# Optimization experiments

Measured on AMD Instinct MI355X. Metric: run time of the kernel, lower is better.

Reference implementation:

```python
import jax, jax.numpy as jnp
import numpy as np

B, L, D, O = 4, 256, 512, 128

def setup_inputs() -> dict:
    key = jax.random.key(0)
    k1, k2, k3, k4, k5, k6 = jax.random.split(key, 6)
    return {
        "x1": jax.random.normal(k1, (B, L, D), jnp.float32),
        "x2": jax.random.normal(k2, (B, L, D), jnp.float32),
        "bw": jax.random.uniform(k3, (2,), jnp.float32),
        "W_bil": jax.random.normal(k4, (O, D + 1, D + 1), jnp.float32) * 0.02,
        "W_lin": jax.random.normal(k5, (2 * D, O), jnp.float32) * 0.02,
        "b_lin": jax.random.normal(k6, (O,), jnp.float32) * 0.02,
    }

def reference(x1, x2, bw, W_bil, W_lin, b_lin):
    bwn = jax.nn.softmax(bw)
    d1 = x1.shape[-1]
    # Bilinear with bias_x/bias_y: append ones column to x1 and x2.
    ones1 = jnp.ones((*x1.shape[:2], 1), x1.dtype)
    ones2 = jnp.ones((*x2.shape[:2], 1), x2.dtype)
    x1b = jnp.concatenate([x1, ones1], axis=-1)  # [B, L1, D+1]
    x2b = jnp.concatenate([x2, ones2], axis=-1)  # [B, L2, D+1]
    # einsum 'bxi,oij,byj->boxy' then permute(0,2,3,1) -> bxyo
    bilinear_logits = jnp.einsum('bxi,oij,byj->bxyo', x1b, W_bil, x2b)
    # linear over concat([x1 expanded, x2 expanded]) == split-weight broadcast sum
    lin1 = x1 @ W_lin[:d1]   # [B, L1, O]
    lin2 = x2 @ W_lin[d1:]   # [B, L2, O]
    linear_logits = lin1[:, :, None, :] + lin2[:, None, :, :] + b_lin  # [B, L1, L2, O]
    return bwn[0] * bilinear_logits + bwn[1] * linear_logits
```

## Files before the change

### kernel.cpp

```cpp
#include <hip/hip_runtime.h>


#define LL 256
#define DD 512
#define OO 128
#define BB 4
#define WB_OI 263169
#define WB_R512 262656

typedef __attribute__((ext_vector_type(8))) short  short8;
typedef __attribute__((ext_vector_type(8))) unsigned short us8;
typedef __attribute__((ext_vector_type(4))) unsigned short us4;
typedef __attribute__((ext_vector_type(4))) float  f32x4;

__device__ __forceinline__ unsigned short f2bf(float f) {
    unsigned int u = __builtin_bit_cast(unsigned int, f);
    u = (u + 0x7FFFu + ((u >> 16) & 1u)) >> 16;
    return (unsigned short)u;
}
__device__ __forceinline__ float bf2f(unsigned short s) {
    return __builtin_bit_cast(float, (unsigned int)s << 16);
}
__device__ __forceinline__ void load_lds16(const void* g, void* l) {
    __builtin_amdgcn_global_load_lds(
        (const __attribute__((address_space(1))) unsigned int*)g,
        (__attribute__((address_space(3))) unsigned int*)l, 16, 0, 0);
}

__global__ __launch_bounds__(256) void cast2_kernel(
    const float* __restrict__ x1, const float* __restrict__ x2,
    unsigned short* __restrict__ x1b, unsigned short* __restrict__ x2b)
{
    int i = blockIdx.x * 256 + threadIdx.x;
    const float* s; unsigned short* d; int j;
    if (i < 131072) { s = x1; d = x1b; j = i; }
    else            { s = x2; d = x2b; j = i - 131072; }
    float4 v = ((const float4*)s)[j];
    us4 u; u.x = f2bf(v.x); u.y = f2bf(v.y); u.z = f2bf(v.z); u.w = f2bf(v.w);
    *(us4*)(d + (size_t)j * 4) = u;
}

__global__ __launch_bounds__(256) void prepw_kernel(
    const float* __restrict__ Wb, const float* __restrict__ bw,
    unsigned short* __restrict__ Wb16)
{
    const int t = threadIdx.x;
    const int row = blockIdx.x * 4 + (t >> 6);
    const int o = row >> 9, i = row & 511;
    const int l = t & 63;
    const float e0 = __expf(bw[0]), e1 = __expf(bw[1]);
    const float bwn0 = e0 / (e0 + e1);
    const float* src = Wb + (size_t)o * WB_OI + (size_t)i * 513;
    unsigned short* dst = Wb16 + (size_t)row * 512;
    float v[8];
    #pragma unroll
    for (int e = 0; e < 8; ++e) v[e] = src[e * 64 + l];
    #pragma unroll
    for (int e = 0; e < 8; ++e) dst[e * 64 + l] = f2bf(bwn0 * v[e]);
}

__global__ __launch_bounds__(256) void prep512_kernel(
    const float* __restrict__ Wb, float* __restrict__ W512T)
{
    int idx = blockIdx.x * 256 + threadIdx.x;
    if (idx < 513 * 128) {
        const int o = idx & 127, j = idx >> 7;
        W512T[idx] = Wb[(size_t)o * WB_OI + WB_R512 + j];
    }
}

__global__ __launch_bounds__(128) void u512_kernel(
    const float* __restrict__ x2, const float* __restrict__ W512T,
    const float* __restrict__ W_lin, const float* __restrict__ b_lin,
    const float* __restrict__ bw, float* __restrict__ u512buf)
{
    __shared__ float xs[DD];
    const int by = blockIdx.x;
    const int o  = threadIdx.x;
    const float* xr = x2 + (size_t)by * DD;
    for (int j = o; j < DD; j += 128) xs[j] = xr[j];
    __syncthreads();
    float s1 = W512T[512 * 128 + o];
    float s2 = b_lin[o];
    #pragma unroll 4
    for (int j = 0; j < DD; ++j) {
        s1 += xs[j] * W512T[j * 128 + o];
        s2 += xs[j] * W_lin[(size_t)(DD + j) * OO + o];
    }
    const float e0 = __expf(bw[0]), e1 = __expf(bw[1]);
    const float bwn0 = e0 / (e0 + e1), bwn1 = e1 / (e0 + e1);
    u512buf[(size_t)by * OO + o] = bwn0 * s1 + bwn1 * s2;
}

__global__ __launch_bounds__(256) void passA_kernel(
    const unsigned short* __restrict__ x2b, const unsigned short* __restrict__ Wb16,
    const float* __restrict__ W_bil, const float* __restrict__ W_lin,
    const float* __restrict__ bw, unsigned short* __restrict__ Up)
{
    __shared__ __align__(16) char smem[33280];
    unsigned short* As0 = (unsigned short*)smem;
    unsigned short* Bs0 = (unsigned short*)(smem + 8192);
    unsigned short* As1 = (unsigned short*)(smem + 16384);
    unsigned short* Bs1 = (unsigned short*)(smem + 24576);
    unsigned short* Cs  = (unsigned short*)smem;
    float* corr = (float*)(smem + 32768);

    const int t = threadIdx.x, w = t >> 6, l = t & 63;
    const int ib = blockIdx.x * 128;
    const int yg = blockIdx.y * 128;
    const int o  = blockIdx.z;
    const int wy = w & 1, wx = w >> 1;

    f32x4 acc[4][4] = {};
    const unsigned short* Wo16 = Wb16 + (size_t)o * DD * DD;

    const int rb0 = w * 32;
    const int rr  = l >> 2;
    const int kof = (l & 3) * 8;

#define STAGE_A(ASP, BSP, K0) do {                                              \
    _Pragma("unroll")                                                           \
    for (int q = 0; q < 2; ++q) {                                               \
        const int rb = rb0 + q * 16, rrow = rb + rr, ko = (K0) + kof;           \
        load_lds16(x2b  + (size_t)(yg + rrow) * DD + ko, (ASP) + rb * 32);      \
        load_lds16(Wo16 + (size_t)(ib + rrow) * DD + ko, (BSP) + rb * 32);      \
    } } while (0)

    STAGE_A(As0, Bs0, 0);
    __syncthreads();

    const int mrow = wy * 64 + (l & 15);
    const int ncol = wx * 64 + (l & 15);
    const int kg = (l >> 4) * 8;

    #pragma unroll 2
    for (int kt = 0; kt < 16; ++kt) {
        const int cur = kt & 1;
        unsigned short* Asr = cur ? As1 : As0;
        unsigned short* Bsr = cur ? Bs1 : Bs0;
        unsigned short* Asn = cur ? As0 : As1;
        unsigned short* Bsn = cur ? Bs0 : Bs1;
        if (kt < 15) STAGE_A(Asn, Bsn, (kt + 1) * 32);
        short8 af[4], bfr[4];
        #pragma unroll
        for (int mt = 0; mt < 4; ++mt) af[mt]  = *(const short8*)(Asr + (mrow + mt * 16) * 32 + kg);
        #pragma unroll
        for (int nt = 0; nt < 4; ++nt) bfr[nt] = *(const short8*)(Bsr + (ncol + nt * 16) * 32 + kg);
        #pragma unroll
        for (int mt = 0; mt < 4; ++mt)
            #pragma unroll
            for (int nt = 0; nt < 4; ++nt)
                acc[mt][nt] = __builtin_amdgcn_mfma_f32_16x16x32_bf16(af[mt], bfr[nt], acc[mt][nt], 0, 0, 0);
        __syncthreads();
    }
#undef STAGE_A

    const float e0 = __expf(bw[0]), e1 = __expf(bw[1]);
    const float bwn0 = e0 / (e0 + e1), bwn1 = e1 / (e0 + e1);
    if (t < 128) {
        const int ig = ib + t;
        corr[t] = bwn1 * W_lin[(size_t)ig * OO + o]
                + bwn0 * W_bil[(size_t)o * WB_OI + (size_t)ig * 513 + 512];
    }
    #pragma unroll
    for (int half = 0; half < 2; ++half) {
        if (wy == half) {
            #pragma unroll
            for (int mt = 0; mt < 4; ++mt) {
                const int yl = mt * 16 + ((l >> 4) << 2);
                #pragma unroll
                for (int nt = 0; nt < 4; ++nt) {
                    const int ic = wx * 64 + nt * 16 + (l & 15);
                    #pragma unroll
                    for (int r = 0; r < 4; ++r)
                        Cs[(yl + r) * 136 + ic] = f2bf(acc[mt][nt][r]);
                }
            }
        }
        __syncthreads();
        #pragma unroll
        for (int p = 0; p < 4; ++p) {
            const int yl = p * 16 + (t >> 4);
            const int i0 = (t & 15) * 8;
            short8 v = *(const short8*)(Cs + yl * 136 + i0);
            us8 uo;
            #pragma unroll
            for (int e = 0; e < 8; ++e)
                uo[e] = f2bf(bf2f((unsigned short)v[e]) + corr[i0 + e]);
            *(us8*)(Up + ((size_t)(yg + half * 64 + yl) * OO + o) * DD + ib + i0) = uo;
        }
        __syncthreads();
    }
}

__global__ __launch_bounds__(256) void passB_kernel(
    const unsigned short* __restrict__ x1b, const unsigned short* __restrict__ Up,
    const float* __restrict__ u512buf, float* __restrict__ out)
{
    __shared__ __align__(16) char smem[33280];
    unsigned short* As0 = (unsigned short*)smem;
    unsigned short* Bs0 = (unsigned short*)(smem + 8192);
    unsigned short* As1 = (unsigned short*)(smem + 16384);
    unsigned short* Bs1 = (unsigned short*)(smem + 24576);
    float* u5 = (float*)(smem + 32768);

    const int t = threadIdx.x, w = t >> 6, l = t & 63;
    const int xb = blockIdx.x * 128;
    const int yg = blockIdx.y;
    const int bb = yg >> 8, y = yg & 255;
    const int wy = w & 1, wx = w >> 1;
    if (t < 128) u5[t] = u512buf[(size_t)yg * OO + t];

    f32x4 acc[4][4] = {};

    const int rb0 = w * 32;
    const int rr  = l >> 2;
    const int kof = (l & 3) * 8;

#define STAGE_B(ASP, BSP, K0) do {                                                   \
    _Pragma("unroll")                                                                \
    for (int q = 0; q < 2; ++q) {                                                    \
        const int rb = rb0 + q * 16, rrow = rb + rr, ko = (K0) + kof;                \
        load_lds16(x1b + (size_t)(bb * LL + xb + rrow) * DD + ko, (ASP) + rb * 32);  \
        load_lds16(Up  + (size_t)(yg * OO + rrow) * DD + ko,      (BSP) + rb * 32);  \
    } } while (0)

    STAGE_B(As0, Bs0, 0);
    __syncthreads();

    const int mrow = wy * 64 + (l & 15);
    const int ncol = wx * 64 + (l & 15);
    const int kg = (l >> 4) * 8;

    #pragma unroll 2
    for (int kt = 0; kt < 16; ++kt) {
        const int cur = kt & 1;
        unsigned short* Asr = cur ? As1 : As0;
        unsigned short* Bsr = cur ? Bs1 : Bs0;
        unsigned short* Asn = cur ? As0 : As1;
        unsigned short* Bsn = cur ? Bs0 : Bs1;
        if (kt < 15) STAGE_B(Asn, Bsn, (kt + 1) * 32);
        short8 af[4], bfr[4];
        #pragma unroll
        for (int mt = 0; mt < 4; ++mt) af[mt]  = *(const short8*)(Asr + (mrow + mt * 16) * 32 + kg);
        #pragma unroll
        for (int nt = 0; nt < 4; ++nt) bfr[nt] = *(const short8*)(Bsr + (ncol + nt * 16) * 32 + kg);
        #pragma unroll
        for (int mt = 0; mt < 4; ++mt)
            #pragma unroll
            for (int nt = 0; nt < 4; ++nt)
                acc[mt][nt] = __builtin_amdgcn_mfma_f32_16x16x32_bf16(af[mt], bfr[nt], acc[mt][nt], 0, 0, 0);
        __syncthreads();
    }
#undef STAGE_B

    #pragma unroll
    for (int mt = 0; mt < 4; ++mt) {
        const int xr = wy * 64 + mt * 16 + ((l >> 4) << 2);
        #pragma unroll
        for (int nt = 0; nt < 4; ++nt) {
            const int oc = wx * 64 + nt * 16 + (l & 15);
            const float c = u5[oc];
            #pragma unroll
            for (int r = 0; r < 4; ++r)
                out[((size_t)(bb * LL + xb + xr + r) * LL + y) * OO + oc] = acc[mt][nt][r] + c;
        }
    }
}

extern "C" void kernel_launch(void* const* d_in, const int* in_sizes, int n_in,
                              void* d_out, int out_size, void* d_ws, size_t ws_size,
                              hipStream_t stream)
{
    const float* x1    = (const float*)d_in[0];
    const float* x2    = (const float*)d_in[1];
    const float* bw    = (const float*)d_in[2];
    const float* W_bil = (const float*)d_in[3];
    const float* W_lin = (const float*)d_in[4];
    const float* b_lin = (const float*)d_in[5];
    float* out = (float*)d_out;

    char* ws = (char*)d_ws;
    unsigned short* x1b16 = (unsigned short*)ws;
    unsigned short* x2b16 = (unsigned short*)(ws + (1u << 20));
    float*          u512b = (float*)(ws + (2u << 20));
    float*          W512T = (float*)(ws + (2u << 20) + (512u << 10));
    unsigned short* Wb16  = (unsigned short*)(ws + (3u << 20));
    unsigned short* Up    = (unsigned short*)(ws + (3u << 20) + ((size_t)128 * 512 * 512 * 2));

    cast2_kernel<<<1024, 256, 0, stream>>>(x1, x2, x1b16, x2b16);
    prepw_kernel<<<16384, 256, 0, stream>>>(W_bil, bw, Wb16);
    prep512_kernel<<<257, 256, 0, stream>>>(W_bil, W512T);
    u512_kernel<<<BB * LL, 128, 0, stream>>>(x2, W512T, W_lin, b_lin, bw, u512b);

    passA_kernel<<<dim3(4, 8, OO), 256, 0, stream>>>(x2b16, Wb16, W_bil, W_lin, bw, Up);
    passB_kernel<<<dim3(2, BB * LL), 256, 0, stream>>>(x1b16, Up, u512b, out);
}
```

Measured before the change: 479.8 us.

## Quad-buffer GEMM pipelines with swizzled LDS, setprio, and XCD-aware block remap

```diff
diff --git a/kernel.cpp b/kernel.cpp
--- a/kernel.cpp
+++ b/kernel.cpp
@@ -97,18 +97,16 @@
     const float* __restrict__ W_bil, const float* __restrict__ W_lin,
     const float* __restrict__ bw, unsigned short* __restrict__ Up)
 {
-    __shared__ __align__(16) char smem[33280];
-    unsigned short* As0 = (unsigned short*)smem;
-    unsigned short* Bs0 = (unsigned short*)(smem + 8192);
-    unsigned short* As1 = (unsigned short*)(smem + 16384);
-    unsigned short* Bs1 = (unsigned short*)(smem + 24576);
+    __shared__ __align__(16) char smem[65536];
     unsigned short* Cs  = (unsigned short*)smem;
-    float* corr = (float*)(smem + 32768);
+    float* corr = (float*)(smem + 17408);
 
     const int t = threadIdx.x, w = t >> 6, l = t & 63;
-    const int ib = blockIdx.x * 128;
-    const int yg = blockIdx.y * 128;
-    const int o  = blockIdx.z;
+    const int id  = blockIdx.x;
+    const int lin = (id & 7) * 512 + (id >> 3);
+    const int o   = lin >> 5;
+    const int ib  = (lin & 3) * 128;
+    const int yg  = ((lin >> 2) & 7) * 128;
     const int wy = w & 1, wx = w >> 1;
 
     f32x4 acc[4][4] = {};
@@ -116,45 +114,60 @@
 
     const int rb0 = w * 32;
     const int rr  = l >> 2;
-    const int kof = (l & 3) * 8;
-
-#define STAGE_A(ASP, BSP, K0) do {                                              \
+    const int kof = ((l & 3) ^ ((l >> 3) & 3)) * 8;
+
+#define STAGE_A(S, K0) do {                                                     \
+    unsigned short* As_ = (unsigned short*)(smem + (S) * 16384);                \
+    unsigned short* Bs_ = As_ + 4096;                                           \
     _Pragma("unroll")                                                           \
     for (int q = 0; q < 2; ++q) {                                               \
         const int rb = rb0 + q * 16, rrow = rb + rr, ko = (K0) + kof;           \
-        load_lds16(x2b  + (size_t)(yg + rrow) * DD + ko, (ASP) + rb * 32);      \
-        load_lds16(Wo16 + (size_t)(ib + rrow) * DD + ko, (BSP) + rb * 32);      \
+        load_lds16(x2b  + (size_t)(yg + rrow) * DD + ko, As_ + rb * 32);        \
+        load_lds16(Wo16 + (size_t)(ib + rrow) * DD + ko, Bs_ + rb * 32);        \
     } } while (0)
 
-    STAGE_A(As0, Bs0, 0);
-    __syncthreads();
+    STAGE_A(0, 0); STAGE_A(1, 32); STAGE_A(2, 64);
 
     const int mrow = wy * 64 + (l & 15);
     const int ncol = wx * 64 + (l & 15);
-    const int kg = (l >> 4) * 8;
-
-    #pragma unroll 2
-    for (int kt = 0; kt < 16; ++kt) {
-        const int cur = kt & 1;
-        unsigned short* Asr = cur ? As1 : As0;
-        unsigned short* Bsr = cur ? Bs1 : Bs0;
-        unsigned short* Asn = cur ? As0 : As1;
-        unsigned short* Bsn = cur ? Bs0 : Bs1;
-        if (kt < 15) STAGE_A(Asn, Bsn, (kt + 1) * 32);
-        short8 af[4], bfr[4];
-        #pragma unroll
-        for (int mt = 0; mt < 4; ++mt) af[mt]  = *(const short8*)(Asr + (mrow + mt * 16) * 32 + kg);
-        #pragma unroll
-        for (int nt = 0; nt < 4; ++nt) bfr[nt] = *(const short8*)(Bsr + (ncol + nt * 16) * 32 + kg);
-        #pragma unroll
-        for (int mt = 0; mt < 4; ++mt)
-            #pragma unroll
-            for (int nt = 0; nt < 4; ++nt)
-                acc[mt][nt] = __builtin_amdgcn_mfma_f32_16x16x32_bf16(af[mt], bfr[nt], acc[mt][nt], 0, 0, 0);
-        __syncthreads();
-    }
+    const int psel = ((l >> 4) ^ ((l >> 1) & 3)) * 8;
+
+#define COMPUTE_T(S) do {                                                       \
+    const unsigned short* As_ = (const unsigned short*)(smem + (S) * 16384);    \
+    const unsigned short* Bs_ = As_ + 4096;                                     \
+    short8 af[4], bfr[4];                                                       \
+    _Pragma("unroll")                                                           \
+    for (int mt = 0; mt < 4; ++mt) af[mt]  = *(const short8*)(As_ + (mrow + mt * 16) * 32 + psel); \
+    _Pragma("unroll")                                                           \
+    for (int nt = 0; nt < 4; ++nt) bfr[nt] = *(const short8*)(Bs_ + (ncol + nt * 16) * 32 + psel); \
+    __builtin_amdgcn_s_setprio(1);                                              \
+    _Pragma("unroll")                                                           \
+    for (int mt = 0; mt < 4; ++mt)                                              \
+        _Pragma("unroll")                                                       \
+        for (int nt = 0; nt < 4; ++nt)                                          \
+            acc[mt][nt] = __builtin_amdgcn_mfma_f32_16x16x32_bf16(af[mt], bfr[nt], acc[mt][nt], 0, 0, 0); \
+    __builtin_amdgcn_s_setprio(0);                                              \
+  } while (0)
+
+    #pragma unroll
+    for (int kt = 0; kt < 14; ++kt) {
+        asm volatile("s_waitcnt vmcnt(8)" ::: "memory");
+        __builtin_amdgcn_s_barrier();
+        asm volatile("" ::: "memory");
+        if (kt < 13) STAGE_A((kt + 3) & 3, (kt + 3) * 32);
+        COMPUTE_T(kt & 3);
+    }
+    asm volatile("s_waitcnt vmcnt(4)" ::: "memory");
+    __builtin_amdgcn_s_barrier();
+    asm volatile("" ::: "memory");
+    COMPUTE_T(2);
+    asm volatile("s_waitcnt vmcnt(0)" ::: "memory");
+    __builtin_amdgcn_s_barrier();
+    asm volatile("" ::: "memory");
+    COMPUTE_T(3);
 #undef STAGE_A
 
+    __syncthreads();
     const float e0 = __expf(bw[0]), e1 = __expf(bw[1]);
     const float bwn0 = e0 / (e0 + e1), bwn1 = e1 / (e0 + e1);
     if (t < 128) {
@@ -197,61 +210,52 @@
     const unsigned short* __restrict__ x1b, const unsigned short* __restrict__ Up,
     const float* __restrict__ u512buf, float* __restrict__ out)
 {
-    __shared__ __align__(16) char smem[33280];
-    unsigned short* As0 = (unsigned short*)smem;
-    unsigned short* Bs0 = (unsigned short*)(smem + 8192);
-    unsigned short* As1 = (unsigned short*)(smem + 16384);
-    unsigned short* Bs1 = (unsigned short*)(smem + 24576);
-    float* u5 = (float*)(smem + 32768);
+    __shared__ __align__(16) char smem[65536];
 
     const int t = threadIdx.x, w = t >> 6, l = t & 63;
     const int xb = blockIdx.x * 128;
     const int yg = blockIdx.y;
     const int bb = yg >> 8, y = yg & 255;
     const int wy = w & 1, wx = w >> 1;
-    if (t < 128) u5[t] = u512buf[(size_t)yg * OO + t];
 
     f32x4 acc[4][4] = {};
 
     const int rb0 = w * 32;
     const int rr  = l >> 2;
-    const int kof = (l & 3) * 8;
-
-#define STAGE_B(ASP, BSP, K0) do {                                                   \
+    const int kof = ((l & 3) ^ ((l >> 3) & 3)) * 8;
+
+#define STAGE_B(S, K0) do {                                                          \
+    unsigned short* As_ = (unsigned short*)(smem + (S) * 16384);                     \
+    unsigned short* Bs_ = As_ + 4096;                                                \
     _Pragma("unroll")                                                                \
     for (int q = 0; q < 2; ++q) {                                                    \
         const int rb = rb0 + q * 16, rrow = rb + rr, ko = (K0) + kof;                \
-        load_lds16(x1b + (size_t)(bb * LL + xb + rrow) * DD + ko, (ASP) + rb * 32);  \
-        load_lds16(Up  + (size_t)(yg * OO + rrow) * DD + ko,      (BSP) + rb * 32);  \
+        load_lds16(x1b + (size_t)(bb * LL + xb + rrow) * DD + ko, As_ + rb * 32);    \
+        load_lds16(Up  + (size_t)(yg * OO + rrow) * DD + ko,      Bs_ + rb * 32);    \
     } } while (0)
 
-    STAGE_B(As0, Bs0, 0);
-    __syncthreads();
+    STAGE_B(0, 0); STAGE_B(1, 32); STAGE_B(2, 64);
 
     const int mrow = wy * 64 + (l & 15);
     const int ncol = wx * 64 + (l & 15);
-    const int kg = (l >> 4) * 8;
-
-    #pragma unroll 2
-    for (int kt = 0; kt < 16; ++kt) {
-        const int cur = kt & 1;
-        unsigned short* Asr = cur ? As1 : As0;
-        unsigned short* Bsr = cur ? Bs1 : Bs0;
-        unsigned short* Asn = cur ? As0 : As1;
-        unsigned short* Bsn = cur ? Bs0 : Bs1;
-        if (kt < 15) STAGE_B(Asn, Bsn, (kt + 1) * 32);
-        short8 af[4], bfr[4];
-        #pragma unroll
-        for (int mt = 0; mt < 4; ++mt) af[mt]  = *(const short8*)(Asr + (mrow + mt * 16) * 32 + kg);
-        #pragma unroll
-        for (int nt = 0; nt < 4; ++nt) bfr[nt] = *(const short8*)(Bsr + (ncol + nt * 16) * 32 + kg);
-        #pragma unroll
-        for (int mt = 0; mt < 4; ++mt)
-            #pragma unroll
-            for (int nt = 0; nt < 4; ++nt)
-                acc[mt][nt] = __builtin_amdgcn_mfma_f32_16x16x32_bf16(af[mt], bfr[nt], acc[mt][nt], 0, 0, 0);
-        __syncthreads();
-    }
+    const int psel = ((l >> 4) ^ ((l >> 1) & 3)) * 8;
+
+    #pragma unroll
+    for (int kt = 0; kt < 14; ++kt) {
+        asm volatile("s_waitcnt vmcnt(8)" ::: "memory");
+        __builtin_amdgcn_s_barrier();
+        asm volatile("" ::: "memory");
+        if (kt < 13) STAGE_B((kt + 3) & 3, (kt + 3) * 32);
+        COMPUTE_T(kt & 3);
+    }
+    asm volatile("s_waitcnt vmcnt(4)" ::: "memory");
+    __builtin_amdgcn_s_barrier();
+    asm volatile("" ::: "memory");
+    COMPUTE_T(2);
+    asm volatile("s_waitcnt vmcnt(0)" ::: "memory");
+    __builtin_amdgcn_s_barrier();
+    asm volatile("" ::: "memory");
+    COMPUTE_T(3);
 #undef STAGE_B
 
     #pragma unroll
@@ -260,7 +264,7 @@
         #pragma unroll
         for (int nt = 0; nt < 4; ++nt) {
             const int oc = wx * 64 + nt * 16 + (l & 15);
-            const float c = u5[oc];
+            const float c = u512buf[(size_t)yg * OO + oc];
             #pragma unroll
             for (int r = 0; r < 4; ++r)
                 out[((size_t)(bb * LL + xb + xr + r) * LL + y) * OO + oc] = acc[mt][nt][r] + c;
@@ -293,6 +297,6 @@
     prep512_kernel<<<257, 256, 0, stream>>>(W_bil, W512T);
     u512_kernel<<<BB * LL, 128, 0, stream>>>(x2, W512T, W_lin, b_lin, bw, u512b);
 
-    passA_kernel<<<dim3(4, 8, OO), 256, 0, stream>>>(x2b16, Wb16, W_bil, W_lin, bw, Up);
+    passA_kernel<<<4096, 256, 0, stream>>>(x2b16, Wb16, W_bil, W_lin, bw, Up);
     passB_kernel<<<dim3(2, BB * LL), 256, 0, stream>>>(x1b16, Up, u512b, out);
 }
```

Result: no change. 488.5 us (+1.8%).

## Swizzle LDS tiles, remap passA block order, retile passB to 256x64

Applied to the files above, without the earlier changes.

```diff
diff --git a/kernel.cpp b/kernel.cpp
--- a/kernel.cpp
+++ b/kernel.cpp
@@ -106,9 +106,11 @@
     float* corr = (float*)(smem + 32768);
 
     const int t = threadIdx.x, w = t >> 6, l = t & 63;
-    const int ib = blockIdx.x * 128;
-    const int yg = blockIdx.y * 128;
-    const int o  = blockIdx.z;
+    const int id  = blockIdx.x;
+    const int lin = (id & 7) * 512 + (id >> 3);
+    const int o   = lin >> 5;
+    const int ib  = (lin & 3) * 128;
+    const int yg  = ((lin >> 2) & 7) * 128;
     const int wy = w & 1, wx = w >> 1;
 
     f32x4 acc[4][4] = {};
@@ -116,14 +118,15 @@
 
     const int rb0 = w * 32;
     const int rr  = l >> 2;
-    const int kof = (l & 3) * 8;
-
-#define STAGE_A(ASP, BSP, K0) do {                                              \
+    const int csw = ((l & 3) ^ (rr & 3)) * 8;
+
+#define STAGE_A(AS_, BS_, K0) do {                                              \
     _Pragma("unroll")                                                           \
     for (int q = 0; q < 2; ++q) {                                               \
-        const int rb = rb0 + q * 16, rrow = rb + rr, ko = (K0) + kof;           \
-        load_lds16(x2b  + (size_t)(yg + rrow) * DD + ko, (ASP) + rb * 32);      \
-        load_lds16(Wo16 + (size_t)(ib + rrow) * DD + ko, (BSP) + rb * 32);      \
+        const int rb = rb0 + q * 16;                                            \
+        const int grow = rb + rr;                                               \
+        load_lds16(x2b  + (size_t)(yg + grow) * DD + (K0) + csw, (AS_) + rb * 32); \
+        load_lds16(Wo16 + (size_t)(ib + grow) * DD + (K0) + csw, (BS_) + rb * 32); \
     } } while (0)
 
     STAGE_A(As0, Bs0, 0);
@@ -131,7 +134,7 @@
 
     const int mrow = wy * 64 + (l & 15);
     const int ncol = wx * 64 + (l & 15);
-    const int kg = (l >> 4) * 8;
+    const int psel = ((l >> 4) ^ (l & 3)) * 8;
 
     #pragma unroll 2
     for (int kt = 0; kt < 16; ++kt) {
@@ -143,9 +146,9 @@
         if (kt < 15) STAGE_A(Asn, Bsn, (kt + 1) * 32);
         short8 af[4], bfr[4];
         #pragma unroll
-        for (int mt = 0; mt < 4; ++mt) af[mt]  = *(const short8*)(Asr + (mrow + mt * 16) * 32 + kg);
-        #pragma unroll
-        for (int nt = 0; nt < 4; ++nt) bfr[nt] = *(const short8*)(Bsr + (ncol + nt * 16) * 32 + kg);
+        for (int mt = 0; mt < 4; ++mt) af[mt]  = *(const short8*)(Asr + (mrow + mt * 16) * 32 + psel);
+        #pragma unroll
+        for (int nt = 0; nt < 4; ++nt) bfr[nt] = *(const short8*)(Bsr + (ncol + nt * 16) * 32 + psel);
         #pragma unroll
         for (int mt = 0; mt < 4; ++mt)
             #pragma unroll
@@ -197,54 +200,50 @@
     const unsigned short* __restrict__ x1b, const unsigned short* __restrict__ Up,
     const float* __restrict__ u512buf, float* __restrict__ out)
 {
-    __shared__ __align__(16) char smem[33280];
-    unsigned short* As0 = (unsigned short*)smem;
-    unsigned short* Bs0 = (unsigned short*)(smem + 8192);
-    unsigned short* As1 = (unsigned short*)(smem + 16384);
-    unsigned short* Bs1 = (unsigned short*)(smem + 24576);
-    float* u5 = (float*)(smem + 32768);
+    __shared__ __align__(16) char smem[40960];
 
     const int t = threadIdx.x, w = t >> 6, l = t & 63;
-    const int xb = blockIdx.x * 128;
+    const int ob = blockIdx.x;
     const int yg = blockIdx.y;
     const int bb = yg >> 8, y = yg & 255;
-    const int wy = w & 1, wx = w >> 1;
-    if (t < 128) u5[t] = u512buf[(size_t)yg * OO + t];
 
     f32x4 acc[4][4] = {};
-
-    const int rb0 = w * 32;
+    const unsigned short* Abase = x1b + (size_t)bb * LL * DD;
+    const unsigned short* Bbase = Up + ((size_t)yg * OO + ob * 64) * DD;
+
     const int rr  = l >> 2;
-    const int kof = (l & 3) * 8;
-
-#define STAGE_B(ASP, BSP, K0) do {                                                   \
-    _Pragma("unroll")                                                                \
-    for (int q = 0; q < 2; ++q) {                                                    \
-        const int rb = rb0 + q * 16, rrow = rb + rr, ko = (K0) + kof;                \
-        load_lds16(x1b + (size_t)(bb * LL + xb + rrow) * DD + ko, (ASP) + rb * 32);  \
-        load_lds16(Up  + (size_t)(yg * OO + rrow) * DD + ko,      (BSP) + rb * 32);  \
-    } } while (0)
-
-    STAGE_B(As0, Bs0, 0);
+    const int csw = ((l & 3) ^ (rr & 3)) * 8;
+
+#define STAGE_B(S, K0) do {                                                     \
+    unsigned short* As_ = (unsigned short*)(smem + (S) * 20480);                \
+    unsigned short* Bs_ = As_ + 8192;                                           \
+    _Pragma("unroll")                                                           \
+    for (int q = 0; q < 4; ++q) {                                               \
+        const int seg = q * 4 + w;                          \
+        load_lds16(Abase + (size_t)(seg * 16 + rr) * DD + (K0) + csw,           \
+                   As_ + seg * 512);                                            \
+    }                                                                           \
+    load_lds16(Bbase + (size_t)(w * 16 + rr) * DD + (K0) + csw, Bs_ + w * 512); \
+  } while (0)
+
+    STAGE_B(0, 0);
     __syncthreads();
 
-    const int mrow = wy * 64 + (l & 15);
-    const int ncol = wx * 64 + (l & 15);
-    const int kg = (l >> 4) * 8;
+    const int mrow = w * 64 + (l & 15);
+    const int ncol = l & 15;
+    const int psel = ((l >> 4) ^ (l & 3)) * 8;
 
     #pragma unroll 2
     for (int kt = 0; kt < 16; ++kt) {
         const int cur = kt & 1;
-        unsigned short* Asr = cur ? As1 : As0;
-        unsigned short* Bsr = cur ? Bs1 : Bs0;
-        unsigned short* Asn = cur ? As0 : As1;
-        unsigned short* Bsn = cur ? Bs0 : Bs1;
-        if (kt < 15) STAGE_B(Asn, Bsn, (kt + 1) * 32);
+        if (kt < 15) STAGE_B(cur ^ 1, (kt + 1) * 32);
+        const unsigned short* As_ = (const unsigned short*)(smem + cur * 20480);
+        const unsigned short* Bs_ = As_ + 8192;
         short8 af[4], bfr[4];
         #pragma unroll
-        for (int mt = 0; mt < 4; ++mt) af[mt]  = *(const short8*)(Asr + (mrow + mt * 16) * 32 + kg);
-        #pragma unroll
-        for (int nt = 0; nt < 4; ++nt) bfr[nt] = *(const short8*)(Bsr + (ncol + nt * 16) * 32 + kg);
+        for (int mt = 0; mt < 4; ++mt) af[mt]  = *(const short8*)(As_ + (mrow + mt * 16) * 32 + psel);
+        #pragma unroll
+        for (int nt = 0; nt < 4; ++nt) bfr[nt] = *(const short8*)(Bs_ + (ncol + nt * 16) * 32 + psel);
         #pragma unroll
         for (int mt = 0; mt < 4; ++mt)
             #pragma unroll
@@ -255,15 +254,15 @@
 #undef STAGE_B
 
     #pragma unroll
-    for (int mt = 0; mt < 4; ++mt) {
-        const int xr = wy * 64 + mt * 16 + ((l >> 4) << 2);
-        #pragma unroll
-        for (int nt = 0; nt < 4; ++nt) {
-            const int oc = wx * 64 + nt * 16 + (l & 15);
-            const float c = u5[oc];
+    for (int nt = 0; nt < 4; ++nt) {
+        const int oc = ob * 64 + nt * 16 + (l & 15);
+        const float c = u512buf[(size_t)yg * OO + oc];
+        #pragma unroll
+        for (int mt = 0; mt < 4; ++mt) {
+            const int xr = w * 64 + mt * 16 + ((l >> 4) << 2);
             #pragma unroll
             for (int r = 0; r < 4; ++r)
-                out[((size_t)(bb * LL + xb + xr + r) * LL + y) * OO + oc] = acc[mt][nt][r] + c;
+                out[((size_t)(bb * LL + xr + r) * LL + y) * OO + oc] = acc[mt][nt][r] + c;
         }
     }
 }
@@ -293,6 +292,6 @@
     prep512_kernel<<<257, 256, 0, stream>>>(W_bil, W512T);
     u512_kernel<<<BB * LL, 128, 0, stream>>>(x2, W512T, W_lin, b_lin, bw, u512b);
 
-    passA_kernel<<<dim3(4, 8, OO), 256, 0, stream>>>(x2b16, Wb16, W_bil, W_lin, bw, Up);
+    passA_kernel<<<4096, 256, 0, stream>>>(x2b16, Wb16, W_bil, W_lin, bw, Up);
     passB_kernel<<<dim3(2, BB * LL), 256, 0, stream>>>(x1b16, Up, u512b, out);
 }
```

New measurement: 510.2 us. 6.3% more time.
